# Optimization experiments

Hardware: AMD Instinct MI355X
Metric: run time of the kernel (lower is better)

Reference implementation:

```python
import jax, jax.numpy as jnp
import numpy as np


def _fo_pool(f, z):
    # c_t = f_t * c_{t-1} + z_t, c_0 = 0, scanned over axis 1 (seq).
    # Associative combine: (a1,b1) * (a2,b2) = (a1*a2, a2*b1 + b2)
    def combine(left, right):
        a1, b1 = left
        a2, b2 = right
        return a1 * a2, a2 * b1 + b2
    _, c = jax.lax.associative_scan(combine, (f, z), axis=1)
    return c


def setup_inputs() -> dict:
    key = jax.random.key(0)
    ks = jax.random.split(key, 10)
    B, S, D_in, D_model, D_mlp, n_cls = 32, 2048, 512, 1024, 1024, 128
    s = 0.02
    return {
        "x":  jax.random.normal(ks[0], (B, S, D_in), dtype=jnp.float32),
        "W":  jax.random.normal(ks[1], (D_in, 3 * D_model), dtype=jnp.float32) * s,  # Linear, bias=False
        "V":  jax.random.normal(ks[2], (D_in, 3 * D_model), dtype=jnp.float32) * s,
        "Vb": jax.random.normal(ks[3], (3 * D_model,), dtype=jnp.float32) * s,
        "W0": jax.random.normal(ks[4], (D_model, D_mlp), dtype=jnp.float32) * s,
        "b0": jax.random.normal(ks[5], (D_mlp,), dtype=jnp.float32) * s,
        "W1": jax.random.normal(ks[6], (D_mlp, D_mlp), dtype=jnp.float32) * s,
        "b1": jax.random.normal(ks[7], (D_mlp,), dtype=jnp.float32) * s,
        "W2": jax.random.normal(ks[8], (D_mlp, n_cls), dtype=jnp.float32) * s,
        "b2": jax.random.normal(ks[9], (n_cls,), dtype=jnp.float32) * s,
    }


def reference(x, W, V, Vb, W0, b0, W1, b1, W2, b2):
    # kernel_size=2 pre: W(x) + V(x shifted right by one, zero-padded)
    xprev = jnp.pad(x[:, :-1, :], ((0, 0), (1, 0), (0, 0)))  # [B,S,D_in]
    pre = jnp.einsum('bsd,dk->bsk', x, W) + jnp.einsum('bsd,dk->bsk', xprev, V) + Vb
    f, z, o = jnp.split(pre, 3, axis=-1)
    f = jax.nn.sigmoid(f)
    z = (1.0 - f) * jnp.tanh(z)
    o = jax.nn.sigmoid(o)
    c = _fo_pool(f, z)          # [B,S,D_model]
    h = c * o
    q = h[:, -1, :]             # last timestep
    # dropout is identity at inference (training=False)
    q = jax.nn.relu(q @ W0 + b0)
    q = jax.nn.relu(q @ W1 + b1)
    return q @ W2 + b2
```

## Files before the change

### kernel.cpp

```cpp
#include <hip/hip_runtime.h>
#include <cstdint>
#include <cstddef>


typedef __attribute__((ext_vector_type(8))) short short8;
typedef __attribute__((ext_vector_type(4))) float f32x4;

#define ZERO_OFF_E 6291456u
#define XB_OFF_E   8388608u

__device__ __forceinline__ unsigned short f2bf(float f) {
  unsigned int u = __float_as_uint(f);
  u += 0x7fffu + ((u >> 16) & 1u);
  return (unsigned short)(u >> 16);
}

__device__ __forceinline__ void gload_lds16(const void* g, void* l) {
  __builtin_amdgcn_global_load_lds(
      (const __attribute__((address_space(1))) unsigned int*)g,
      (__attribute__((address_space(3))) unsigned int*)l, 16, 0, 0);
}

__device__ __forceinline__ float sigmoidf_fast(float x) {
  return 1.f / (1.f + __expf(-x));
}
__device__ __forceinline__ float tanhf_fast(float x) {
  float a = fabsf(x);
  float e = __expf(-2.f * a);
  float t = (1.f - e) / (1.f + e);
  return copysignf(t, x);
}

__global__ void prologue_kernel(const float* __restrict__ x, const float* __restrict__ W,
                                const float* __restrict__ V,
                                const float* __restrict__ b0, const float* __restrict__ b1,
                                const float* __restrict__ b2,
                                unsigned short* __restrict__ xb, unsigned short* __restrict__ U,
                                float* __restrict__ q0, float* __restrict__ q1,
                                float* __restrict__ out) {
  __shared__ float T[64 * 65];
  const int bx = blockIdx.x;
  if (bx < 32768) {
    int gid = bx * 256 + threadIdx.x;
    float4 v = ((const float4*)x)[gid];
    ushort4 o;
    o.x = f2bf(v.x); o.y = f2bf(v.y); o.z = f2bf(v.z); o.w = f2bf(v.w);
    ((ushort4*)xb)[gid] = o;
  } else if (bx < 33280) {
    const int u = bx - 32768;
    const int j0 = (u & 31) * 64;
    const int k0 = (u >> 5) * 64;
    const int jl = threadIdx.x & 63;
    const int q  = threadIdx.x >> 6;
    const float* src = (k0 < 512) ? (W + (size_t)k0 * 3072) : (V + (size_t)(k0 - 512) * 3072);
#pragma unroll 4
    for (int i = 0; i < 16; ++i) {
      int kl = q * 16 + i;
      T[kl * 65 + jl] = src[(size_t)kl * 3072 + j0 + jl];
    }
    __syncthreads();
    const int kl = threadIdx.x & 63;
#pragma unroll 4
    for (int i = 0; i < 16; ++i) {
      int jj = q * 16 + i;
      U[(size_t)(j0 + jj) * 1024 + k0 + kl] = f2bf(T[kl * 65 + jj]);
    }
  } else {
    int gid = (bx - 33280) * 256 + threadIdx.x;
    q0[gid] = b0[gid & 1023];
    q1[gid] = b1[gid & 1023];
    if (gid < 4096) out[gid] = b2[gid & 127];
  }
}

template <bool USE_BF>
__global__ __launch_bounds__(512, 4) void qrnn_main(
    const unsigned short* __restrict__ wsb, const float* __restrict__ xf,
    const float* __restrict__ Vb,
    float* __restrict__ Fagg, float* __restrict__ Zagg) {
  __shared__ __align__(16) char smem[65664];
  char* As = smem;
  char* Us = smem + 32896;

  const int dt = blockIdx.x;
  const int cj = blockIdx.y;
  const int b  = blockIdx.z;
  const int tid = threadIdx.x;
  const int lane = tid & 63;
  const int wid  = tid >> 6;
  const int wm = wid >> 1, wn = wid & 1;
  const int s0 = cj * 256;

  f32x4 acc[4][4];
#pragma unroll
  for (int i = 0; i < 4; ++i)
#pragma unroll
    for (int j = 0; j < 4; ++j) acc[i][j] = f32x4{0.f, 0.f, 0.f, 0.f};

  const int mrow = wm * 64 + (lane & 15);
  const int ncol = wn * 64 + (lane & 15);
  const int rloc = lane >> 3;
  const int pc   = lane & 7;
  const int c0   = lane >> 4;

  unsigned voffA[4], voffU[4];
  unsigned voffA4 = 0;
#pragma unroll
  for (int p = 0; p < 4; ++p) {
    int rr = wid * 32 + p * 8 + rloc;
    int c = pc ^ (rr & 7);
    int sg = s0 - 1 + rr;
    voffA[p] = (sg >= 0)
        ? (XB_OFF_E + (unsigned)(b * 2048 + sg) * 512u + (unsigned)(c * 8))
        : (ZERO_OFF_E + (unsigned)(pc * 8));
    int half = rr >> 7, col = rr & 127;
    int j = (col < 64) ? (dt * 64 + col) : (1024 + dt * 64 + (col - 64));
    voffU[p] = (unsigned)(j * 1024 + half * 512 + c * 8);
  }
  if (tid < 8)
    voffA4 = XB_OFF_E + (unsigned)(b * 2048 + s0 + 255) * 512u + (unsigned)(tid * 8);

  const char* pA[2][2];
  const char* pU[2];
#pragma unroll
  for (int h2 = 0; h2 < 2; ++h2) {
    int rr = mrow + 1 - h2;
#pragma unroll
    for (int kb = 0; kb < 2; ++kb)
      pA[h2][kb] = As + rr * 128 + (((kb * 4 + c0) ^ (rr & 7)) << 4);
  }
#pragma unroll
  for (int kb = 0; kb < 2; ++kb)
    pU[kb] = Us + ncol * 128 + (((kb * 4 + c0) ^ (ncol & 7)) << 4);

  const unsigned short* base = wsb;

#pragma unroll
  for (int kt = 0; kt < 8; ++kt) {
    __syncthreads();
    if constexpr (USE_BF) {
#pragma unroll
      for (int p = 0; p < 4; ++p)
        gload_lds16(base + voffA[p], As + (wid * 32 + p * 8) * 128);
      if (tid < 8)
        gload_lds16(base + voffA4, As + 256 * 128);
#pragma unroll
      for (int p = 0; p < 4; ++p)
        gload_lds16(base + voffU[p], Us + (wid * 32 + p * 8) * 128);
    } else {
#pragma unroll
      for (int p = 0; p < 4; ++p) {
        int rr = (tid >> 3) + p * 64;
        int fc = tid & 7;
        int s = s0 - 1 + rr;
        uint4 v = make_uint4(0u, 0u, 0u, 0u);
        if (s >= 0) {
          const float* src = xf + (((size_t)b * 2048 + s) << 9) + kt * 64 + fc * 8;
          float4 a0 = *(const float4*)src;
          float4 a1 = *(const float4*)(src + 4);
          v.x = (unsigned)f2bf(a0.x) | ((unsigned)f2bf(a0.y) << 16);
          v.y = (unsigned)f2bf(a0.z) | ((unsigned)f2bf(a0.w) << 16);
          v.z = (unsigned)f2bf(a1.x) | ((unsigned)f2bf(a1.y) << 16);
          v.w = (unsigned)f2bf(a1.z) | ((unsigned)f2bf(a1.w) << 16);
        }
        *(uint4*)(As + rr * 128 + ((fc ^ (rr & 7)) << 4)) = v;
      }
      if (tid < 8) {
        const float* src = xf + (((size_t)b * 2048 + s0 + 255) << 9) + kt * 64 + tid * 8;
        float4 a0 = *(const float4*)src;
        float4 a1 = *(const float4*)(src + 4);
        uint4 v;
        v.x = (unsigned)f2bf(a0.x) | ((unsigned)f2bf(a0.y) << 16);
        v.y = (unsigned)f2bf(a0.z) | ((unsigned)f2bf(a0.w) << 16);
        v.z = (unsigned)f2bf(a1.x) | ((unsigned)f2bf(a1.y) << 16);
        v.w = (unsigned)f2bf(a1.z) | ((unsigned)f2bf(a1.w) << 16);
        *(uint4*)(As + 256 * 128 + (tid << 4)) = v;
      }
#pragma unroll
      for (int p = 0; p < 4; ++p) {
        int fc = tid & 7;
        uint4 v = *(const uint4*)(wsb + voffU[p] + kt * 64);
        *(uint4*)(Us + (wid * 32 + p * 8 + rloc) * 128 + (((fc ^ ((wid * 32 + p * 8 + rloc) & 7)) ^ (pc ^ ((wid * 32 + p * 8 + rloc) & 7))) << 4) + (pc << 4)) = v;
      }
    }
    __syncthreads();
#pragma unroll
    for (int h2 = 0; h2 < 2; ++h2) {
#pragma unroll
      for (int kb = 0; kb < 2; ++kb) {
        const char* pa = pA[h2][kb];
        const char* pu = pU[kb] + h2 * 16384;
        short8 bfr[4];
#pragma unroll
        for (int nt = 0; nt < 4; ++nt)
          bfr[nt] = *(const short8*)(pu + nt * 2048);
#pragma unroll
        for (int mt = 0; mt < 4; ++mt) {
          short8 afr = *(const short8*)(pa + mt * 2048);
#pragma unroll
          for (int nt = 0; nt < 4; ++nt)
            acc[mt][nt] = __builtin_amdgcn_mfma_f32_16x16x32_bf16(afr, bfr[nt], acc[mt][nt], 0, 0, 0);
        }
      }
    }
    base += 64;
  }

  float* fA   = (float*)smem;
  float* tzA  = (float*)(smem + 17408);
  float* segF = (float*)(smem + 34816);
  float* segZ = (float*)(smem + 36864);

  const int d = tid & 63;
  const int dl = lane & 15;
  float vb[4];
#pragma unroll
  for (int nt = 0; nt < 4; ++nt)
    vb[nt] = Vb[wn * 1024 + dt * 64 + nt * 16 + dl];

  float F_run = 1.f, Z_run = 0.f;

  for (int ph = 0; ph < 4; ++ph) {
    __syncthreads();
    if (wm == ph) {
      float* dst = (wn == 0) ? fA : tzA;
#pragma unroll
      for (int mt = 0; mt < 4; ++mt)
#pragma unroll
        for (int nt = 0; nt < 4; ++nt)
#pragma unroll
          for (int rg = 0; rg < 4; ++rg) {
            int t = mt * 16 + ((lane >> 4) << 2) + rg;
            int c = nt * 16 + dl;
            float v = acc[mt][nt][rg] + vb[nt];
            v = (wn == 0) ? sigmoidf_fast(v) : tanhf_fast(v);
            dst[t * 68 + c] = v;
          }
    }
    __syncthreads();
    {
      int seg = tid >> 6;
      float F = 1.f, Z = 0.f;
#pragma unroll
      for (int i = 0; i < 8; ++i) {
        int t = seg * 8 + i;
        float f  = fA[t * 68 + d];
        float tz = tzA[t * 68 + d];
        float z = (1.f - f) * tz;
        Z = f * Z + z;
        F *= f;
      }
      segF[seg * 64 + d] = F;
      segZ[seg * 64 + d] = Z;
    }
    __syncthreads();
    if (tid < 64) {
#pragma unroll
      for (int sgi = 0; sgi < 8; ++sgi) {
        float Fs = segF[sgi * 64 + tid], Zs = segZ[sgi * 64 + tid];
        Z_run = Fs * Z_run + Zs;
        F_run *= Fs;
      }
    }
  }
  if (tid < 64) {
    size_t o = (((size_t)b * 8 + cj) << 10) + dt * 64 + tid;
    Fagg[o] = F_run;
    Zagg[o] = Z_run;
  }
}

__global__ void head_kernel(const float* __restrict__ x, const float* __restrict__ W,
                            const float* __restrict__ V, const float* __restrict__ Vb,
                            const float* __restrict__ Fagg, const float* __restrict__ Zagg,
                            float* __restrict__ h) {
  __shared__ float red[4][64];
  const int dl = threadIdx.x & 63;
  const int w  = threadIdx.x >> 6;
  const int d = blockIdx.x * 64 + dl;
  const int b = blockIdx.y;

  const float* xl = x + ((size_t)b * 2048 + 2047) * 512;
  const float* xp = xl - 512;
  const float* Wc = W + 2048 + d;
  const float* Vc = V + 2048 + d;
  float po = 0.f;
  const int k0 = w * 128;
#pragma unroll 8
  for (int k = k0; k < k0 + 128; ++k) {
    po += xl[k] * Wc[(size_t)k * 3072];
    po += xp[k] * Vc[(size_t)k * 3072];
  }
  red[w][dl] = po;
  __syncthreads();
  if (w == 0) {
    po = red[0][dl] + red[1][dl] + red[2][dl] + red[3][dl] + Vb[2048 + d];
    float c = 0.f;
#pragma unroll
    for (int j = 0; j < 8; ++j) {
      size_t o = (((size_t)b * 8 + j) << 10) + d;
      c = Fagg[o] * c + Zagg[o];
    }
    h[((size_t)b << 10) + d] = c * sigmoidf_fast(po);
  }
}

__global__ void mlp_atomic_kernel(const float* __restrict__ in, const float* __restrict__ Wt,
                                  float* __restrict__ out, int K, int N, int relu_in) {
  __shared__ float red[4][64];
  const int nl = threadIdx.x & 63;
  const int w  = threadIdx.x >> 6;
  const int n = blockIdx.x * 64 + nl;
  const int b = blockIdx.y;
  const int k0 = blockIdx.z * (K >> 2) + w * (K >> 4);
  const float* row = in + (size_t)b * K;
  const float* Wc = Wt + n;
  float s = 0.f;
#pragma unroll 8
  for (int k = k0; k < k0 + (K >> 4); ++k) {
    float v = row[k];
    if (relu_in) v = fmaxf(v, 0.f);
    s += v * Wc[(size_t)k * N];
  }
  red[w][nl] = s;
  __syncthreads();
  if (w == 0) {
    s = red[0][nl] + red[1][nl] + red[2][nl] + red[3][nl];
    atomicAdd(&out[(size_t)b * N + n], s);
  }
}

extern "C" void kernel_launch(void* const* d_in, const int* in_sizes, int n_in,
                              void* d_out, int out_size, void* d_ws, size_t ws_size,
                              hipStream_t stream) {
  const float* x  = (const float*)d_in[0];
  const float* W  = (const float*)d_in[1];
  const float* V  = (const float*)d_in[2];
  const float* Vb = (const float*)d_in[3];
  const float* W0 = (const float*)d_in[4];
  const float* b0 = (const float*)d_in[5];
  const float* W1 = (const float*)d_in[6];
  const float* b1 = (const float*)d_in[7];
  const float* W2 = (const float*)d_in[8];
  const float* b2 = (const float*)d_in[9];

  char* ws = (char*)d_ws;
  unsigned short* U = (unsigned short*)(ws);
  float* Fagg = (float*)(ws + (size_t)4 * 1024 * 1024);
  float* Zagg = (float*)(ws + (size_t)6 * 1024 * 1024);
  float* h    = (float*)(ws + (size_t)8 * 1024 * 1024);
  float* q0   = (float*)(ws + (size_t)8 * 1024 * 1024 + 256 * 1024);
  float* q1   = (float*)(ws + (size_t)8 * 1024 * 1024 + 512 * 1024);
  char*  zpg  = ws + (size_t)12 * 1024 * 1024;
  unsigned short* xb = (unsigned short*)(ws + (size_t)16 * 1024 * 1024);

  const size_t need_bf = (size_t)16 * 1024 * 1024 + (size_t)67108864;
  int use_bf = (ws_size >= need_bf) ? 1 : 0;

  hipMemsetAsync(zpg, 0, 4096, stream);
  prologue_kernel<<<33408, 256, 0, stream>>>(x, W, V, b0, b1, b2, xb, U, q0, q1,
                                             (float*)d_out);
  if (use_bf)
    qrnn_main<true><<<dim3(16, 8, 32), 512, 0, stream>>>((const unsigned short*)ws, x,
                                                         Vb, Fagg, Zagg);
  else
    qrnn_main<false><<<dim3(16, 8, 32), 512, 0, stream>>>((const unsigned short*)ws, x,
                                                          Vb, Fagg, Zagg);
  head_kernel<<<dim3(16, 32), 256, 0, stream>>>(x, W, V, Vb, Fagg, Zagg, h);
  mlp_atomic_kernel<<<dim3(16, 32, 4), 256, 0, stream>>>(h, W0, q0, 1024, 1024, 0);
  mlp_atomic_kernel<<<dim3(16, 32, 4), 256, 0, stream>>>(q0, W1, q1, 1024, 1024, 1);
  mlp_atomic_kernel<<<dim3(2, 32, 4), 256, 0, stream>>>(q1, W2, (float*)d_out, 1024, 128, 1);
}
```

Before: 665.9 us.

## Shrink QRNN GEMM tiles and prefetch next K-slice through registers

The main QRNN kernel now uses 256-thread blocks covering 128 timesteps instead of 512 threads over 256, doubling the grid and cutting shared memory so more blocks fit per CU. The direct global-to-LDS loads are replaced by register prefetch of the next 32-wide K stage, stored to padded LDS rows after a barrier so global latency overlaps the MFMA work. The chunk aggregates grow from 8 to 16 per batch, and the head kernel's combine is updated to match. The separate memset of the zero page is folded into an extra prologue block to save a launch. The trade-off is twice as many barrier pairs per K pass, and each block does less work relative to its fixed prologue and scan overhead.

```diff
diff --git a/kernel.cpp b/kernel.cpp
--- a/kernel.cpp
+++ b/kernel.cpp
@@ -13,12 +13,6 @@
   unsigned int u = __float_as_uint(f);
   u += 0x7fffu + ((u >> 16) & 1u);
   return (unsigned short)(u >> 16);
-}
-
-__device__ __forceinline__ void gload_lds16(const void* g, void* l) {
-  __builtin_amdgcn_global_load_lds(
-      (const __attribute__((address_space(1))) unsigned int*)g,
-      (__attribute__((address_space(3))) unsigned int*)l, 16, 0, 0);
 }
 
 __device__ __forceinline__ float sigmoidf_fast(float x) {
@@ -37,7 +31,7 @@
                                 const float* __restrict__ b2,
                                 unsigned short* __restrict__ xb, unsigned short* __restrict__ U,
                                 float* __restrict__ q0, float* __restrict__ q1,
-                                float* __restrict__ out) {
+                                float* __restrict__ out, uint4* __restrict__ zpg) {
   __shared__ float T[64 * 65];
   const int bx = blockIdx.x;
   if (bx < 32768) {
@@ -65,22 +59,22 @@
       int jj = q * 16 + i;
       U[(size_t)(j0 + jj) * 1024 + k0 + kl] = f2bf(T[kl * 65 + jj]);
     }
-  } else {
+  } else if (bx < 33408) {
     int gid = (bx - 33280) * 256 + threadIdx.x;
     q0[gid] = b0[gid & 1023];
     q1[gid] = b1[gid & 1023];
     if (gid < 4096) out[gid] = b2[gid & 127];
+  } else {
+    zpg[threadIdx.x] = make_uint4(0u, 0u, 0u, 0u);
   }
 }
 
 template <bool USE_BF>
-__global__ __launch_bounds__(512, 4) void qrnn_main(
+__global__ __launch_bounds__(256, 3) void qrnn_main(
     const unsigned short* __restrict__ wsb, const float* __restrict__ xf,
     const float* __restrict__ Vb,
     float* __restrict__ Fagg, float* __restrict__ Zagg) {
-  __shared__ __align__(16) char smem[65664];
-  char* As = smem;
-  char* Us = smem + 32896;
+  __shared__ __align__(16) char smem[36864];
 
   const int dt = blockIdx.x;
   const int cj = blockIdx.y;
@@ -89,7 +83,8 @@
   const int lane = tid & 63;
   const int wid  = tid >> 6;
   const int wm = wid >> 1, wn = wid & 1;
-  const int s0 = cj * 256;
+  const int s0 = cj * 128;
+  const int l15 = lane & 15, lc = lane >> 4;
 
   f32x4 acc[4][4];
 #pragma unroll
@@ -97,130 +92,141 @@
 #pragma unroll
     for (int j = 0; j < 4; ++j) acc[i][j] = f32x4{0.f, 0.f, 0.f, 0.f};
 
-  const int mrow = wm * 64 + (lane & 15);
-  const int ncol = wn * 64 + (lane & 15);
-  const int rloc = lane >> 3;
-  const int pc   = lane & 7;
-  const int c0   = lane >> 4;
-
-  unsigned voffA[4], voffU[4];
-  unsigned voffA4 = 0;
-#pragma unroll
-  for (int p = 0; p < 4; ++p) {
-    int rr = wid * 32 + p * 8 + rloc;
-    int c = pc ^ (rr & 7);
-    int sg = s0 - 1 + rr;
-    voffA[p] = (sg >= 0)
-        ? (XB_OFF_E + (unsigned)(b * 2048 + sg) * 512u + (unsigned)(c * 8))
-        : (ZERO_OFF_E + (unsigned)(pc * 8));
-    int half = rr >> 7, col = rr & 127;
+  unsigned voffA[2];
+  size_t offAF[2]; int zAF[2];
+#pragma unroll
+  for (int p = 0; p < 2; ++p) {
+    int cw = tid + p * 256;
+    int r = cw >> 2, c = cw & 3;
+    int sg = s0 - 1 + r;
+    voffA[p] = (sg < 0) ? (ZERO_OFF_E + (unsigned)(c * 8))
+                        : (XB_OFF_E + (unsigned)(b * 2048 + sg) * 512u + (unsigned)(c * 8));
+    zAF[p] = (sg < 0);
+    offAF[p] = ((size_t)(b * 2048 + (sg < 0 ? 0 : sg)) << 9) + c * 8;
+  }
+  unsigned voffA3 = XB_OFF_E + (unsigned)(b * 2048 + s0 + 127) * 512u + (unsigned)((tid & 3) * 8);
+  size_t offAF3 = ((size_t)(b * 2048 + s0 + 127) << 9) + (tid & 3) * 8;
+
+  unsigned voffU[4];
+#pragma unroll
+  for (int k = 0; k < 4; ++k) {
+    int uw = tid + k * 256;
+    int r = uw >> 2, c = uw & 3;
+    int col = r & 127, half = r >> 7;
     int j = (col < 64) ? (dt * 64 + col) : (1024 + dt * 64 + (col - 64));
-    voffU[p] = (unsigned)(j * 1024 + half * 512 + c * 8);
-  }
-  if (tid < 8)
-    voffA4 = XB_OFF_E + (unsigned)(b * 2048 + s0 + 255) * 512u + (unsigned)(tid * 8);
-
-  const char* pA[2][2];
-  const char* pU[2];
+    voffU[k] = (unsigned)(j * 1024 + half * 512 + c * 8);
+  }
+
+  unsigned wA[2], wU[4];
+#pragma unroll
+  for (int p = 0; p < 2; ++p) {
+    int cw = tid + p * 256;
+    wA[p] = (unsigned)((cw >> 2) * 80 + (cw & 3) * 16);
+  }
+  const unsigned wA3 = (unsigned)(128 * 80 + (tid & 3) * 16);
+#pragma unroll
+  for (int k = 0; k < 4; ++k) {
+    int uw = tid + k * 256;
+    wU[k] = (unsigned)(10320 + (uw >> 2) * 80 + (uw & 3) * 16);
+  }
+
+  unsigned roA[2][4], roU[2][4];
 #pragma unroll
   for (int h2 = 0; h2 < 2; ++h2) {
-    int rr = mrow + 1 - h2;
-#pragma unroll
-    for (int kb = 0; kb < 2; ++kb)
-      pA[h2][kb] = As + rr * 128 + (((kb * 4 + c0) ^ (rr & 7)) << 4);
-  }
-#pragma unroll
-  for (int kb = 0; kb < 2; ++kb)
-    pU[kb] = Us + ncol * 128 + (((kb * 4 + c0) ^ (ncol & 7)) << 4);
-
-  const unsigned short* base = wsb;
-
-#pragma unroll
-  for (int kt = 0; kt < 8; ++kt) {
-    __syncthreads();
+#pragma unroll
+    for (int mt = 0; mt < 4; ++mt) {
+      int rr = wm * 64 + l15 + mt * 16 + 1 - h2;
+      roA[h2][mt] = (unsigned)(rr * 80 + lc * 16);
+    }
+#pragma unroll
+    for (int nt = 0; nt < 4; ++nt) {
+      int rrU = h2 * 128 + wn * 64 + l15 + nt * 16;
+      roU[h2][nt] = (unsigned)(10320 + rrU * 80 + lc * 16);
+    }
+  }
+
+  uint4 pA0, pA1, pA3, pU0, pU1, pU2, pU3;
+
+  auto load_stage = [&](int s) {
+    const unsigned short* cur = wsb + s * 32;
     if constexpr (USE_BF) {
-#pragma unroll
-      for (int p = 0; p < 4; ++p)
-        gload_lds16(base + voffA[p], As + (wid * 32 + p * 8) * 128);
-      if (tid < 8)
-        gload_lds16(base + voffA4, As + 256 * 128);
-#pragma unroll
-      for (int p = 0; p < 4; ++p)
-        gload_lds16(base + voffU[p], Us + (wid * 32 + p * 8) * 128);
+      pA0 = *(const uint4*)(cur + voffA[0]);
+      pA1 = *(const uint4*)(cur + voffA[1]);
+      if (tid < 4) pA3 = *(const uint4*)(cur + voffA3);
     } else {
-#pragma unroll
-      for (int p = 0; p < 4; ++p) {
-        int rr = (tid >> 3) + p * 64;
-        int fc = tid & 7;
-        int s = s0 - 1 + rr;
+      const float* curf = xf + s * 32;
+#pragma unroll
+      for (int p = 0; p < 2; ++p) {
         uint4 v = make_uint4(0u, 0u, 0u, 0u);
-        if (s >= 0) {
-          const float* src = xf + (((size_t)b * 2048 + s) << 9) + kt * 64 + fc * 8;
-          float4 a0 = *(const float4*)src;
-          float4 a1 = *(const float4*)(src + 4);
+        if (!zAF[p]) {
+          float4 a0 = *(const float4*)(curf + offAF[p]);
+          float4 a1 = *(const float4*)(curf + offAF[p] + 4);
           v.x = (unsigned)f2bf(a0.x) | ((unsigned)f2bf(a0.y) << 16);
           v.y = (unsigned)f2bf(a0.z) | ((unsigned)f2bf(a0.w) << 16);
           v.z = (unsigned)f2bf(a1.x) | ((unsigned)f2bf(a1.y) << 16);
           v.w = (unsigned)f2bf(a1.z) | ((unsigned)f2bf(a1.w) << 16);
         }
-        *(uint4*)(As + rr * 128 + ((fc ^ (rr & 7)) << 4)) = v;
-      }
-      if (tid < 8) {
-        const float* src = xf + (((size_t)b * 2048 + s0 + 255) << 9) + kt * 64 + tid * 8;
-        float4 a0 = *(const float4*)src;
-        float4 a1 = *(const float4*)(src + 4);
-        uint4 v;
-        v.x = (unsigned)f2bf(a0.x) | ((unsigned)f2bf(a0.y) << 16);
-        v.y = (unsigned)f2bf(a0.z) | ((unsigned)f2bf(a0.w) << 16);
-        v.z = (unsigned)f2bf(a1.x) | ((unsigned)f2bf(a1.y) << 16);
-        v.w = (unsigned)f2bf(a1.z) | ((unsigned)f2bf(a1.w) << 16);
-        *(uint4*)(As + 256 * 128 + (tid << 4)) = v;
-      }
-#pragma unroll
-      for (int p = 0; p < 4; ++p) {
-        int fc = tid & 7;
-        uint4 v = *(const uint4*)(wsb + voffU[p] + kt * 64);
-        *(uint4*)(Us + (wid * 32 + p * 8 + rloc) * 128 + (((fc ^ ((wid * 32 + p * 8 + rloc) & 7)) ^ (pc ^ ((wid * 32 + p * 8 + rloc) & 7))) << 4) + (pc << 4)) = v;
-      }
-    }
-    __syncthreads();
+        if (p == 0) pA0 = v; else pA1 = v;
+      }
+      if (tid < 4) {
+        float4 a0 = *(const float4*)(curf + offAF3);
+        float4 a1 = *(const float4*)(curf + offAF3 + 4);
+        pA3.x = (unsigned)f2bf(a0.x) | ((unsigned)f2bf(a0.y) << 16);
+        pA3.y = (unsigned)f2bf(a0.z) | ((unsigned)f2bf(a0.w) << 16);
+        pA3.z = (unsigned)f2bf(a1.x) | ((unsigned)f2bf(a1.y) << 16);
+        pA3.w = (unsigned)f2bf(a1.z) | ((unsigned)f2bf(a1.w) << 16);
+      }
+    }
+    pU0 = *(const uint4*)(cur + voffU[0]);
+    pU1 = *(const uint4*)(cur + voffU[1]);
+    pU2 = *(const uint4*)(cur + voffU[2]);
+    pU3 = *(const uint4*)(cur + voffU[3]);
+  };
+
+  load_stage(0);
+
+#pragma unroll 1
+  for (int s = 0; s < 16; ++s) {
+    __syncthreads();
+    *(uint4*)(smem + wA[0]) = pA0;
+    *(uint4*)(smem + wA[1]) = pA1;
+    if (tid < 4) *(uint4*)(smem + wA3) = pA3;
+    *(uint4*)(smem + wU[0]) = pU0;
+    *(uint4*)(smem + wU[1]) = pU1;
+    *(uint4*)(smem + wU[2]) = pU2;
+    *(uint4*)(smem + wU[3]) = pU3;
+    __syncthreads();
+    if (s < 15) load_stage(s + 1);
 #pragma unroll
     for (int h2 = 0; h2 < 2; ++h2) {
-#pragma unroll
-      for (int kb = 0; kb < 2; ++kb) {
-        const char* pa = pA[h2][kb];
-        const char* pu = pU[kb] + h2 * 16384;
-        short8 bfr[4];
+      short8 bfr[4];
+#pragma unroll
+      for (int nt = 0; nt < 4; ++nt)
+        bfr[nt] = *(const short8*)(smem + roU[h2][nt]);
+#pragma unroll
+      for (int mt = 0; mt < 4; ++mt) {
+        short8 afr = *(const short8*)(smem + roA[h2][mt]);
 #pragma unroll
         for (int nt = 0; nt < 4; ++nt)
-          bfr[nt] = *(const short8*)(pu + nt * 2048);
-#pragma unroll
-        for (int mt = 0; mt < 4; ++mt) {
-          short8 afr = *(const short8*)(pa + mt * 2048);
-#pragma unroll
-          for (int nt = 0; nt < 4; ++nt)
-            acc[mt][nt] = __builtin_amdgcn_mfma_f32_16x16x32_bf16(afr, bfr[nt], acc[mt][nt], 0, 0, 0);
-        }
-      }
-    }
-    base += 64;
+          acc[mt][nt] = __builtin_amdgcn_mfma_f32_16x16x32_bf16(afr, bfr[nt], acc[mt][nt], 0, 0, 0);
+      }
+    }
   }
 
   float* fA   = (float*)smem;
   float* tzA  = (float*)(smem + 17408);
   float* segF = (float*)(smem + 34816);
-  float* segZ = (float*)(smem + 36864);
+  float* segZ = (float*)(smem + 35840);
 
   const int d = tid & 63;
-  const int dl = lane & 15;
   float vb[4];
 #pragma unroll
   for (int nt = 0; nt < 4; ++nt)
-    vb[nt] = Vb[wn * 1024 + dt * 64 + nt * 16 + dl];
+    vb[nt] = Vb[wn * 1024 + dt * 64 + nt * 16 + l15];
 
   float F_run = 1.f, Z_run = 0.f;
 
-  for (int ph = 0; ph < 4; ++ph) {
+  for (int ph = 0; ph < 2; ++ph) {
     __syncthreads();
     if (wm == ph) {
       float* dst = (wn == 0) ? fA : tzA;
@@ -231,7 +237,7 @@
 #pragma unroll
           for (int rg = 0; rg < 4; ++rg) {
             int t = mt * 16 + ((lane >> 4) << 2) + rg;
-            int c = nt * 16 + dl;
+            int c = nt * 16 + l15;
             float v = acc[mt][nt][rg] + vb[nt];
             v = (wn == 0) ? sigmoidf_fast(v) : tanhf_fast(v);
             dst[t * 68 + c] = v;
@@ -241,9 +247,9 @@
     {
       int seg = tid >> 6;
       float F = 1.f, Z = 0.f;
-#pragma unroll
-      for (int i = 0; i < 8; ++i) {
-        int t = seg * 8 + i;
+#pragma unroll 4
+      for (int i = 0; i < 16; ++i) {
+        int t = seg * 16 + i;
         float f  = fA[t * 68 + d];
         float tz = tzA[t * 68 + d];
         float z = (1.f - f) * tz;
@@ -256,7 +262,7 @@
     __syncthreads();
     if (tid < 64) {
 #pragma unroll
-      for (int sgi = 0; sgi < 8; ++sgi) {
+      for (int sgi = 0; sgi < 4; ++sgi) {
         float Fs = segF[sgi * 64 + tid], Zs = segZ[sgi * 64 + tid];
         Z_run = Fs * Z_run + Zs;
         F_run *= Fs;
@@ -264,7 +270,7 @@
     }
   }
   if (tid < 64) {
-    size_t o = (((size_t)b * 8 + cj) << 10) + dt * 64 + tid;
+    size_t o = (((size_t)b * 16 + cj) << 10) + dt * 64 + tid;
     Fagg[o] = F_run;
     Zagg[o] = Z_run;
   }
@@ -297,8 +303,8 @@
     po = red[0][dl] + red[1][dl] + red[2][dl] + red[3][dl] + Vb[2048 + d];
     float c = 0.f;
 #pragma unroll
-    for (int j = 0; j < 8; ++j) {
-      size_t o = (((size_t)b * 8 + j) << 10) + d;
+    for (int j = 0; j < 16; ++j) {
+      size_t o = (((size_t)b * 16 + j) << 10) + d;
       c = Fagg[o] * c + Zagg[o];
     }
     h[((size_t)b << 10) + d] = c * sigmoidf_fast(po);
@@ -351,21 +357,20 @@
   float* h    = (float*)(ws + (size_t)8 * 1024 * 1024);
   float* q0   = (float*)(ws + (size_t)8 * 1024 * 1024 + 256 * 1024);
   float* q1   = (float*)(ws + (size_t)8 * 1024 * 1024 + 512 * 1024);
-  char*  zpg  = ws + (size_t)12 * 1024 * 1024;
+  uint4* zpg  = (uint4*)(ws + (size_t)12 * 1024 * 1024);
   unsigned short* xb = (unsigned short*)(ws + (size_t)16 * 1024 * 1024);
 
   const size_t need_bf = (size_t)16 * 1024 * 1024 + (size_t)67108864;
   int use_bf = (ws_size >= need_bf) ? 1 : 0;
 
-  hipMemsetAsync(zpg, 0, 4096, stream);
-  prologue_kernel<<<33408, 256, 0, stream>>>(x, W, V, b0, b1, b2, xb, U, q0, q1,
-                                             (float*)d_out);
+  prologue_kernel<<<33409, 256, 0, stream>>>(x, W, V, b0, b1, b2, xb, U, q0, q1,
+                                             (float*)d_out, zpg);
   if (use_bf)
-    qrnn_main<true><<<dim3(16, 8, 32), 512, 0, stream>>>((const unsigned short*)ws, x,
-                                                         Vb, Fagg, Zagg);
+    qrnn_main<true><<<dim3(16, 16, 32), 256, 0, stream>>>((const unsigned short*)ws, x,
+                                                          Vb, Fagg, Zagg);
   else
-    qrnn_main<false><<<dim3(16, 8, 32), 512, 0, stream>>>((const unsigned short*)ws, x,
-                                                          Vb, Fagg, Zagg);
+    qrnn_main<false><<<dim3(16, 16, 32), 256, 0, stream>>>((const unsigned short*)ws, x,
+                                                           Vb, Fagg, Zagg);
   head_kernel<<<dim3(16, 32), 256, 0, stream>>>(x, W, V, Vb, Fagg, Zagg, h);
   mlp_atomic_kernel<<<dim3(16, 32, 4), 256, 0, stream>>>(h, W0, q0, 1024, 1024, 0);
   mlp_atomic_kernel<<<dim3(16, 32, 4), 256, 0, stream>>>(q0, W1, q1, 1024, 1024, 1);
```

Result: faster. 609.5 us (-8.5%).
